# Performance work log

Measured on AMD Instinct MI355X. Metric: run time of the kernel, lower is better.

The kernel has to match this reference:

```python
import jax, jax.numpy as jnp
import numpy as np

B, M, N, T = 16, 16, 32, 80


def setup_inputs() -> dict:
    key = jax.random.key(0)
    ks = jax.random.split(key, 20)
    p = lambda k, shp: jax.random.normal(k, shp, jnp.float32) * 0.05
    return {
        "ego_traj": jax.random.normal(ks[0], (B, M, T, 6), jnp.float32),
        "ego_encoding": jax.random.normal(ks[1], (B, 256), jnp.float32),
        "agents_traj": jax.random.normal(ks[2], (B, M, N, T, 3), jnp.float32),
        "agents_states": jax.random.normal(ks[3], (B, N, 11), jnp.float32),
        # interaction_feature_encoder: Linear(10,64) -> ReLU -> Linear(64,256)
        "enc_w1": p(ks[4], (10, 64)), "enc_b1": p(ks[5], (64,)),
        "enc_w2": p(ks[6], (64, 256)), "enc_b2": p(ks[7], (256,)),
        # interaction_feature_decoder: Linear(256,64) -> ELU -> Linear(64,4) -> Sigmoid
        "dec_w1": p(ks[8], (256, 64)), "dec_b1": p(ks[9], (64,)),
        "dec_w2": p(ks[10], (64, 4)), "dec_b2": p(ks[11], (4,)),
        # weights_decoder: Linear(256,64) -> ELU -> Linear(64,8) -> Softplus
        "wd_w1": p(ks[12], (256, 64)), "wd_b1": p(ks[13], (64,)),
        "wd_w2": p(ks[14], (64, 8)), "wd_b2": p(ks[15], (8,)),
        "timesteps": 80,
    }


def reference(ego_traj, ego_encoding, agents_traj, agents_states,
              enc_w1, enc_b1, enc_w2, enc_b2,
              dec_w1, dec_b1, dec_w2, dec_b2,
              wd_w1, wd_b1, wd_w2, wd_b2, timesteps):
    Tm = timesteps
    # ---- hardcoded ego features: B,M,4 ----
    speed = ego_traj[:, :, :Tm, 3]
    acc = ego_traj[:, :, :Tm, 4]
    jerk = jnp.diff(acc, axis=-1) / 0.1
    jerk = jnp.concatenate([jerk[:, :, :1], jerk], axis=-1)
    curvature = ego_traj[:, :, :Tm, 5]
    lat_acc = speed ** 2 * curvature
    hard = jnp.stack([
        -jnp.clip(speed.mean(-1), 0.0, 15.0) / 15.0,
        jnp.clip(jnp.abs(acc).mean(-1), 0.0, 4.0) / 4.0,
        jnp.clip(jnp.abs(jerk).mean(-1), 0.0, 6.0) / 6.0,
        jnp.clip(jnp.abs(lat_acc).mean(-1), 0.0, 5.0) / 5.0,
    ], axis=-1)  # B,M,4

    # ---- latent interaction features (vectorized over M) ----
    agent_mask = (agents_states.sum(-1) != 0).astype(ego_traj.dtype)  # B,N
    ry = agents_traj[:, :, :, :Tm, 2] - ego_traj[:, :, None, :Tm, 2]  # B,M,N,T
    ry = jnp.arctan2(jnp.sin(ry), jnp.cos(ry))
    rp = agents_traj[:, :, :, :Tm, :2] - ego_traj[:, :, None, :Tm, :2]
    rp = jnp.stack([rp[..., 0] * jnp.cos(ry), rp[..., 1] * jnp.sin(ry)], axis=-1)
    av = jnp.diff(agents_traj[:, :, :, :Tm, :2], axis=-2) / 0.1
    av = jnp.concatenate([av[:, :, :, :1, :], av], axis=-2)
    evx = ego_traj[:, :, :Tm, 3] * jnp.cos(ego_traj[:, :, :Tm, 2])  # B,M,T
    evy = ego_traj[:, :, :Tm, 3] * jnp.sin(ego_traj[:, :, :Tm, 2])
    rv = jnp.stack([(av[..., 0] - evx[:, :, None]) * jnp.cos(ry),
                    (av[..., 1] - evy[:, :, None]) * jnp.sin(ry)], axis=-1)
    rel = jnp.concatenate([rp, ry[..., None], rv], axis=-1)  # B,M,N,T,5
    aattr = jnp.broadcast_to(agents_states[:, None, :, None, 6:], rel.shape[:4] + (5,))
    attr = jnp.concatenate([rel, aattr], axis=-1) * agent_mask[:, None, :, None, None]  # B,M,N,T,10
    h = jax.nn.relu(attr @ enc_w1 + enc_b1) @ enc_w2 + enc_b2  # B,M,N,T,256
    feat = h.max(axis=2).mean(axis=2)  # max over agents, mean over time -> B,M,256
    inter = jax.nn.sigmoid(jax.nn.elu(feat @ dec_w1 + dec_b1) @ dec_w2 + dec_b2)  # B,M,4

    # ---- weights (variable_cost=False -> ones_like encoding) ----
    enc_in = jnp.ones_like(ego_encoding)
    weights = jax.nn.softplus(jax.nn.elu(enc_in @ wd_w1 + wd_b1) @ wd_w2 + wd_b2)  # B,8

    # ---- collision cost: B,M ----
    dist = jnp.linalg.norm(ego_traj[:, :, None, :Tm, :2] - agents_traj[:, :, :, :Tm, :2], axis=-1)
    coll = (jnp.exp(-0.2 * dist ** 2) * agent_mask[:, None, :, None]).sum((-1, -2))

    feats = jnp.concatenate([hard, inter], axis=-1)  # B,M,8
    scores = -jnp.sum(feats * weights[:, None, :], axis=-1) - 10.0 * coll
    ego_mask = ego_traj.sum(-1).sum(-1) != 0  # B,M
    scores = jnp.where(ego_mask, scores, -jnp.inf)
    return scores, weights
```

## Files before the change

### kernel.cpp

```cpp
#include <hip/hip_runtime.h>
#include <hip/hip_fp16.h>
#include <math.h>
#include <string.h>

typedef __attribute__((ext_vector_type(8))) short short8;
typedef __attribute__((ext_vector_type(8))) _Float16 f16x8;
typedef __attribute__((ext_vector_type(4))) _Float16 h4;
typedef __attribute__((ext_vector_type(2))) _Float16 h2;
typedef __attribute__((ext_vector_type(4))) float f32x4;

#define NB 16
#define NM 16
#define NN 32
#define NT 80
#define TC 16
#define NP 5
#define CH 4
#define NCH 8

#define WS_WTS 0
#define WS_BF 16
#define WS_BB 8208
#define WS_BASE 24592
#define WS_BM_STRIDE 1344
#define WS_SC_OFF 1280

__device__ __forceinline__ short f2h(float f) {
  _Float16 h = (_Float16)f;
  short s; memcpy(&s, &h, 2); return s;
}
__device__ __forceinline__ unsigned h2bits(h2 h) {
  unsigned u; memcpy(&u, &h, 4); return u;
}
__device__ __forceinline__ h2 bits2h(unsigned u) {
  h2 h; memcpy(&h, &u, 4); return h;
}

__global__ void prep_kernel(const float* __restrict__ agents_states,
                            const float* __restrict__ enc_w1,
                            const float* __restrict__ enc_b1,
                            const float* __restrict__ enc_w2,
                            const float* __restrict__ wd_w1,
                            const float* __restrict__ wd_b1,
                            const float* __restrict__ wd_w2,
                            const float* __restrict__ wd_b2,
                            float* __restrict__ ws,
                            float* __restrict__ out) {
  const int blk = blockIdx.x;
  const int tid = threadIdx.x;
  if (blk < NB) {
    __shared__ float smask[NN];
    if (tid < NN) {
      const float* st = agents_states + ((size_t)blk * NN + tid) * 11;
      float s = 0.f;
      for (int i = 0; i < 11; ++i) s += st[i];
      smask[tid] = (s != 0.f) ? 1.f : 0.f;
    }
    __syncthreads();
    h2* bb = reinterpret_cast<h2*>(ws + WS_BB) + blk * (NN * 32);
    for (int e = tid; e < NN * 32; e += 256) {
      int n = e >> 5, jp = e & 31;
      const float* st = agents_states + ((size_t)blk * NN + n) * 11 + 6;
      float v[2];
#pragma unroll
      for (int hh = 0; hh < 2; ++hh) {
        int j = jp * 2 + hh;
        float acc = st[0] * enc_w1[5 * 64 + j] + st[1] * enc_w1[6 * 64 + j] +
                    st[2] * enc_w1[7 * 64 + j] + st[3] * enc_w1[8 * 64 + j] +
                    st[4] * enc_w1[9 * 64 + j];
        v[hh] = smask[n] * acc + enc_b1[j];
      }
      h2 r; r[0] = (_Float16)v[0]; r[1] = (_Float16)v[1];
      bb[e] = r;
    }
  } else {
    __shared__ float sh[64];
    if (tid < 64) {
      float acc = wd_b1[tid];
      for (int i = 0; i < 256; ++i) acc += wd_w1[i * 64 + tid];
      sh[tid] = acc > 0.f ? acc : expm1f(acc);
    }
    __syncthreads();
    if (tid < 8) {
      float acc = wd_b2[tid];
      for (int k = 0; k < 64; ++k) acc += sh[k] * wd_w2[k * 8 + tid];
      float sp = log1pf(__expf(acc));
      ws[WS_WTS + tid] = sp;
      for (int b = 0; b < NB; ++b) out[NB * NM + b * 8 + tid] = sp;
    }
    const int g = tid >> 6;
    const int lane = tid & 63;
    short8* bft = reinterpret_cast<short8*>(ws + WS_BF);
#pragma unroll
    for (int q = 0; q < 8; ++q) {
      int s = g * 8 + q;
      int wv = s >> 3, jb = (s >> 1) & 3, kt = s & 1;
      int col = wv * 64 + jb * 16 + (lane & 15);
      int krow = (lane >> 4) * 8;
      short8 v;
#pragma unroll
      for (int j = 0; j < 8; ++j)
        v[j] = f2h(enc_w2[(kt * 32 + krow + j) * 256 + col]);
      bft[s * 64 + lane] = v;
    }
  }
}

__global__ __launch_bounds__(256, 4) void score_partial(
    const float* __restrict__ ego_traj,
    const float* __restrict__ agents_traj,
    const float* __restrict__ agents_states,
    const float* __restrict__ enc_w1,
    float* __restrict__ ws)
{
  __shared__ h4 s_r01[NN][TC];
  __shared__ h4 s_r23[NN][TC];
  __shared__ h2 s_r4[NN][TC];
  __shared__ uint2 s_bb[NN][16];
  __shared__ __align__(16) char s_hid[2][CH][TC * 128];
  __shared__ float s_ego[TC][5];
  __shared__ float s_acc[TC + 2];
  __shared__ float s_spd[TC], s_lat[TC], s_egos[TC];
  __shared__ float s_mask[NN];
  __shared__ float s_cw[4];

  const int p = blockIdx.x;
  const int bm = blockIdx.y;
  const int t0 = p * TC;
  const int b = bm >> 4;
  const int tid = threadIdx.x;
  const int lane = tid & 63;
  const int wv = tid >> 6;

  float* ws_bm = ws + WS_BASE + (size_t)bm * WS_BM_STRIDE;

  if (tid < TC) {
    int i = tid;
    const float* e = ego_traj + ((size_t)bm * NT + (t0 + i)) * 6;
    float ex = e[0], ey = e[1], eh = e[2], spd = e[3], acc = e[4], cur = e[5];
    s_ego[i][0] = ex; s_ego[i][1] = ey; s_ego[i][2] = eh;
    s_ego[i][3] = spd * __cosf(eh);
    s_ego[i][4] = spd * __sinf(eh);
    s_spd[i] = spd;
    s_acc[i + 1] = acc;
    s_lat[i] = fabsf(spd * spd * cur);
    s_egos[i] = ex + ey + eh + spd + acc + cur;
  } else if (tid == TC) {
    int tp = (p == 0) ? 0 : (t0 - 1);
    s_acc[0] = ego_traj[((size_t)bm * NT + tp) * 6 + 4];
  } else if (tid >= 64 && tid < 64 + NN) {
    int n = tid - 64;
    const float* st = agents_states + ((size_t)b * NN + n) * 11;
    float s = 0.f;
    for (int i = 0; i < 11; ++i) s += st[i];
    s_mask[n] = (s != 0.f) ? 1.f : 0.f;
  }
  {
    const uint2* bbt = reinterpret_cast<const uint2*>(ws + WS_BB) + b * 512;
#pragma unroll
    for (int k = 0; k < 2; ++k) {
      int e = tid + k * 256;
      s_bb[e >> 4][e & 15] = bbt[e];
    }
  }

  const int jq = tid & 15;
  const int tt = tid >> 4;
  const int j0 = jq * 4;

  f16x8 Bf[4][2];
  {
    const f16x8* bft = reinterpret_cast<const f16x8*>(ws + WS_BF);
#pragma unroll
    for (int jb = 0; jb < 4; ++jb)
#pragma unroll
      for (int kt = 0; kt < 2; ++kt)
        Bf[jb][kt] = bft[((wv * 4 + jb) * 2 + kt) * 64 + lane];
  }

  h2 w1h[5][2];
#pragma unroll
  for (int f = 0; f < 5; ++f)
#pragma unroll
    for (int jp = 0; jp < 2; ++jp) {
      h2 r;
      r[0] = (_Float16)enc_w1[f * 64 + j0 + jp * 2];
      r[1] = (_Float16)enc_w1[f * 64 + j0 + jp * 2 + 1];
      w1h[f][jp] = r;
    }
  __syncthreads();

  {
    float collacc = 0.f;
    const float* atraj = agents_traj + (size_t)bm * (NN * NT * 3);
#pragma unroll
    for (int k = 0; k < 2; ++k) {
      int pp = tid + k * 256;
      int n = pp >> 4;
      int i = pp & 15;
      int tg = t0 + i;
      const float* bp = atraj + n * (NT * 3) + tg * 3;
      float ax = bp[0], ay = bp[1], ah = bp[2];
      float avx, avy;
      if (tg == 0) { avx = (bp[3] - ax) * 10.f; avy = (bp[4] - ay) * 10.f; }
      else         { avx = (ax - bp[-3]) * 10.f; avy = (ay - bp[-2]) * 10.f; }
      float ex = s_ego[i][0], ey = s_ego[i][1], eh = s_ego[i][2];
      float evx = s_ego[i][3], evy = s_ego[i][4];
      float m = s_mask[n];
      float ryr = ah - eh;
      float w = ryr - 6.283185307179586f * rintf(ryr * 0.15915494309189535f);
      float cy = __cosf(ryr), sy = __sinf(ryr);
      float dx = ax - ex, dy = ay - ey;
      float r0 = dx * cy * m, r1 = dy * sy * m, r2 = w * m;
      float r3 = (avx - evx) * cy * m, r4 = (avy - evy) * sy * m;
      h4 v01, v23; h2 v4;
      v01[0] = v01[1] = (_Float16)r0; v01[2] = v01[3] = (_Float16)r1;
      v23[0] = v23[1] = (_Float16)r2; v23[2] = v23[3] = (_Float16)r3;
      v4[0] = v4[1] = (_Float16)r4;
      s_r01[n][i] = v01;
      s_r23[n][i] = v23;
      s_r4[n][i] = v4;
      collacc += __expf(-0.2f * (dx * dx + dy * dy)) * m;
    }
#pragma unroll
    for (int off = 1; off < 64; off <<= 1) collacc += __shfl_xor(collacc, off);
    if (lane == 0) s_cw[wv] = collacc;
  }

  if (tid >= 251) {
    int which = tid - 251;
    float s = 0.f;
    if (which == 0)      { for (int i = 0; i < TC; ++i) s += s_spd[i]; }
    else if (which == 1) { for (int i = 0; i < TC; ++i) s += fabsf(s_acc[i + 1]); }
    else if (which == 2) {
      for (int i = 0; i < TC; ++i) {
        int ia = (p == 0 && i == 0) ? 2 : (i + 1);
        s += fabsf((s_acc[ia] - s_acc[ia - 1]) * 10.f);
      }
    }
    else if (which == 3) { for (int i = 0; i < TC; ++i) s += s_lat[i]; }
    else                 { for (int i = 0; i < TC; ++i) s += s_egos[i]; }
    ws_bm[WS_SC_OFF + p * 8 + which] = s;
  }

  const int tl = lane & 15, kg = lane >> 4;
  const int swr = (tl & 7) << 4;
  const int aoff0 = tl * 128 + ((kg * 16) ^ swr);
  const int aoff1 = tl * 128 + ((64 + kg * 16) ^ swr);
  const int wbyte = tt * 128 + ((jq * 8) ^ ((tt & 7) << 4));

  h2 z2; z2[0] = z2[1] = (_Float16)0.f;

  auto compute_chunk = [&](int c, int buf) {
#pragma unroll
    for (int nn = 0; nn < CH; ++nn) {
      const int n = c * CH + nn;
      h4 r01 = s_r01[n][tt];
      h4 r23 = s_r23[n][tt];
      h2 r4 = s_r4[n][tt];
      uint2 bb = s_bb[n][jq];
      h2 a0 = __builtin_shufflevector(r01, r01, 0, 1);
      h2 a1 = __builtin_shufflevector(r01, r01, 2, 3);
      h2 a2 = __builtin_shufflevector(r23, r23, 0, 1);
      h2 a3 = __builtin_shufflevector(r23, r23, 2, 3);
      uint2 u;
#pragma unroll
      for (int jp = 0; jp < 2; ++jp) {
        h2 ha = bits2h(jp ? bb.y : bb.x);
        ha = a0 * w1h[0][jp] + ha;
        ha = a1 * w1h[1][jp] + ha;
        ha = a2 * w1h[2][jp] + ha;
        ha = a3 * w1h[3][jp] + ha;
        ha = r4 * w1h[4][jp] + ha;
        ha = __builtin_elementwise_max(ha, z2);
        if (jp == 0) u.x = h2bits(ha); else u.y = h2bits(ha);
      }
      *reinterpret_cast<uint2*>(&s_hid[buf][nn][0] + wbyte) = u;
    }
  };

  f32x4 rmax[4];
#pragma unroll
  for (int jb = 0; jb < 4; ++jb)
    rmax[jb] = f32x4{-3e38f, -3e38f, -3e38f, -3e38f};

  auto mfma_step = [&](int buf) {
#pragma unroll
    for (int nn = 0; nn < CH; ++nn) {
      const char* slab = &s_hid[buf][nn][0];
      f16x8 A0 = *reinterpret_cast<const f16x8*>(slab + aoff0);
      f16x8 A1 = *reinterpret_cast<const f16x8*>(slab + aoff1);
#pragma unroll
      for (int jb = 0; jb < 4; ++jb) {
        f32x4 c = {0.f, 0.f, 0.f, 0.f};
        c = __builtin_amdgcn_mfma_f32_16x16x32_f16(A0, Bf[jb][0], c, 0, 0, 0);
        c = __builtin_amdgcn_mfma_f32_16x16x32_f16(A1, Bf[jb][1], c, 0, 0, 0);
        rmax[jb] = __builtin_elementwise_max(rmax[jb], c);
      }
    }
  };

  __syncthreads();
  compute_chunk(0, 0);
  __syncthreads();

  for (int c = 0; c < NCH; ++c) {
    if (c + 1 < NCH) compute_chunk(c + 1, (c + 1) & 1);
    mfma_step(c & 1);
    __syncthreads();
  }

  {
#pragma unroll
    for (int jb = 0; jb < 4; ++jb) {
      float s = (rmax[jb][0] + rmax[jb][1]) + (rmax[jb][2] + rmax[jb][3]);
      s += __shfl_xor(s, 16);
      s += __shfl_xor(s, 32);
      if (lane < 16)
        ws_bm[p * 256 + wv * 64 + jb * 16 + lane] = s;
    }
  }
  if (tid == 0)
    ws_bm[WS_SC_OFF + p * 8 + 5] = s_cw[0] + s_cw[1] + s_cw[2] + s_cw[3];
}

__global__ void combine_kernel(const float* __restrict__ ws,
                               const float* __restrict__ enc_b2,
                               const float* __restrict__ dec_w1,
                               const float* __restrict__ dec_b1,
                               const float* __restrict__ dec_w2,
                               const float* __restrict__ dec_b2,
                               float* __restrict__ out_scores) {
  __shared__ float s_feat[256];
  __shared__ float s_dh[64];
  __shared__ float s_hard[4];
  __shared__ float s_inter[4];
  __shared__ float s_mc[2];
  const int bm = blockIdx.x;
  const int tid = threadIdx.x;
  const float* wb = ws + WS_BASE + (size_t)bm * WS_BM_STRIDE;

  for (int c = tid; c < 256; c += 64) {
    float f = 0.f;
#pragma unroll
    for (int pp = 0; pp < NP; ++pp) f += wb[pp * 256 + c];
    s_feat[c] = f * (1.f / NT) + enc_b2[c];
  }
  const float* sc = wb + WS_SC_OFF;
  if (tid < 6) {
    float s = 0.f;
#pragma unroll
    for (int pp = 0; pp < NP; ++pp) s += sc[pp * 8 + tid];
    if (tid == 0) s_hard[0] = -fminf(fmaxf(s * (1.f / NT), 0.f), 15.f) * (1.f / 15.f);
    if (tid == 1) s_hard[1] = fminf(fmaxf(s * (1.f / NT), 0.f), 4.f) * 0.25f;
    if (tid == 2) s_hard[2] = fminf(fmaxf(s * (1.f / NT), 0.f), 6.f) * (1.f / 6.f);
    if (tid == 3) s_hard[3] = fminf(fmaxf(s * (1.f / NT), 0.f), 5.f) * 0.2f;
    if (tid == 4) s_mc[0] = s;
    if (tid == 5) s_mc[1] = s;
  }
  __syncthreads();

  {
    float a0 = 0.f, a1 = 0.f, a2 = 0.f, a3 = 0.f;
    for (int i = 0; i < 256; i += 4) {
      a0 += s_feat[i + 0] * dec_w1[(i + 0) * 64 + tid];
      a1 += s_feat[i + 1] * dec_w1[(i + 1) * 64 + tid];
      a2 += s_feat[i + 2] * dec_w1[(i + 2) * 64 + tid];
      a3 += s_feat[i + 3] * dec_w1[(i + 3) * 64 + tid];
    }
    float acc = dec_b1[tid] + ((a0 + a1) + (a2 + a3));
    s_dh[tid] = acc > 0.f ? acc : expm1f(acc);
  }
  __syncthreads();

  if (tid < 4) {
    float acc = dec_b2[tid];
    for (int k = 0; k < 64; ++k) acc += s_dh[k] * dec_w2[k * 4 + tid];
    s_inter[tid] = 1.f / (1.f + __expf(-acc));
  }
  __syncthreads();

  if (tid == 0) {
    const float* wts = ws + WS_WTS;
    float scv = 0.f;
#pragma unroll
    for (int i = 0; i < 4; ++i) scv += s_hard[i] * wts[i];
#pragma unroll
    for (int i = 0; i < 4; ++i) scv += s_inter[i] * wts[4 + i];
    scv = -scv - 10.f * s_mc[1];
    if (s_mc[0] == 0.f) scv = -INFINITY;
    out_scores[bm] = scv;
  }
}

extern "C" void kernel_launch(void* const* d_in, const int* in_sizes, int n_in,
                              void* d_out, int out_size, void* d_ws, size_t ws_size,
                              hipStream_t stream) {
  const float* ego_traj      = (const float*)d_in[0];
  const float* agents_traj   = (const float*)d_in[2];
  const float* agents_states = (const float*)d_in[3];
  const float* enc_w1 = (const float*)d_in[4];
  const float* enc_b1 = (const float*)d_in[5];
  const float* enc_w2 = (const float*)d_in[6];
  const float* enc_b2 = (const float*)d_in[7];
  const float* dec_w1 = (const float*)d_in[8];
  const float* dec_b1 = (const float*)d_in[9];
  const float* dec_w2 = (const float*)d_in[10];
  const float* dec_b2 = (const float*)d_in[11];
  const float* wd_w1 = (const float*)d_in[12];
  const float* wd_b1 = (const float*)d_in[13];
  const float* wd_w2 = (const float*)d_in[14];
  const float* wd_b2 = (const float*)d_in[15];

  float* out = (float*)d_out;
  float* ws = (float*)d_ws;

  prep_kernel<<<NB + 1, 256, 0, stream>>>(agents_states, enc_w1, enc_b1, enc_w2,
                                          wd_w1, wd_b1, wd_w2, wd_b2, ws, out);
  dim3 grid(NP, NB * NM);
  score_partial<<<grid, 256, 0, stream>>>(
      ego_traj, agents_traj, agents_states, enc_w1, ws);
  combine_kernel<<<NB * NM, 64, 0, stream>>>(
      ws, enc_b2, dec_w1, dec_b1, dec_w2, dec_b2, out);
}
```

Baseline: 43.26 us.

## Fuse combine into score kernel via last-block atomic counter; split weight prep

Removes the separate combine kernel launch. Each (b,m) row now has a counter in the workspace that prep zeroes. The last score block to finish for a row runs the decoder MLP and writes the score, reusing shared memory and splitting the 256x64 matvec across four waves. The fp16 repacking of enc_w2 also moves from one prep block into eight extra blocks to shorten the prep critical path. The cost is an atomic, threadfences and a serial tail inside the last block of each row.

```diff
diff --git a/kernel.cpp b/kernel.cpp
--- a/kernel.cpp
+++ b/kernel.cpp
@@ -19,9 +19,10 @@
 #define NCH 8
 
 #define WS_WTS 0
-#define WS_BF 16
-#define WS_BB 8208
-#define WS_BASE 24592
+#define WS_CNT 8
+#define WS_BF 264
+#define WS_BB 8456
+#define WS_BASE 24840
 #define WS_BM_STRIDE 1344
 #define WS_SC_OFF 1280
 
@@ -49,6 +50,8 @@
   const int blk = blockIdx.x;
   const int tid = threadIdx.x;
   if (blk < NB) {
+    if (tid < 16)
+      reinterpret_cast<unsigned*>(ws + WS_CNT)[blk * 16 + tid] = 0u;
     __shared__ float smask[NN];
     if (tid < NN) {
       const float* st = agents_states + ((size_t)blk * NN + tid) * 11;
@@ -73,6 +76,18 @@
       h2 r; r[0] = (_Float16)v[0]; r[1] = (_Float16)v[1];
       bb[e] = r;
     }
+  } else if (blk < NB + 8) {
+    const int g = tid >> 6;
+    const int lane = tid & 63;
+    const int s = (blk - NB) * 4 + g;
+    const int wv = s >> 3, jb = (s >> 1) & 3, kt = s & 1;
+    const int col = wv * 64 + jb * 16 + (lane & 15);
+    const int krow = (lane >> 4) * 8;
+    short8 v;
+#pragma unroll
+    for (int j = 0; j < 8; ++j)
+      v[j] = f2h(enc_w2[(kt * 32 + krow + j) * 256 + col]);
+    reinterpret_cast<short8*>(ws + WS_BF)[s * 64 + lane] = v;
   } else {
     __shared__ float sh[64];
     if (tid < 64) {
@@ -88,21 +103,6 @@
       ws[WS_WTS + tid] = sp;
       for (int b = 0; b < NB; ++b) out[NB * NM + b * 8 + tid] = sp;
     }
-    const int g = tid >> 6;
-    const int lane = tid & 63;
-    short8* bft = reinterpret_cast<short8*>(ws + WS_BF);
-#pragma unroll
-    for (int q = 0; q < 8; ++q) {
-      int s = g * 8 + q;
-      int wv = s >> 3, jb = (s >> 1) & 3, kt = s & 1;
-      int col = wv * 64 + jb * 16 + (lane & 15);
-      int krow = (lane >> 4) * 8;
-      short8 v;
-#pragma unroll
-      for (int j = 0; j < 8; ++j)
-        v[j] = f2h(enc_w2[(kt * 32 + krow + j) * 256 + col]);
-      bft[s * 64 + lane] = v;
-    }
   }
 }
 
@@ -111,7 +111,11 @@
     const float* __restrict__ agents_traj,
     const float* __restrict__ agents_states,
     const float* __restrict__ enc_w1,
-    float* __restrict__ ws)
+    const float* __restrict__ enc_b2,
+    const float* __restrict__ dec_w1, const float* __restrict__ dec_b1,
+    const float* __restrict__ dec_w2, const float* __restrict__ dec_b2,
+    float* __restrict__ ws,
+    float* __restrict__ out_scores)
 {
   __shared__ h4 s_r01[NN][TC];
   __shared__ h4 s_r23[NN][TC];
@@ -123,6 +127,8 @@
   __shared__ float s_spd[TC], s_lat[TC], s_egos[TC];
   __shared__ float s_mask[NN];
   __shared__ float s_cw[4];
+  __shared__ int s_last;
+  __shared__ float s_hard[4], s_inter[4], s_mc[2];
 
   const int p = blockIdx.x;
   const int bm = blockIdx.y;
@@ -133,6 +139,7 @@
   const int wv = tid >> 6;
 
   float* ws_bm = ws + WS_BASE + (size_t)bm * WS_BM_STRIDE;
+  unsigned* cnt_bm = reinterpret_cast<unsigned*>(ws + WS_CNT) + bm;
 
   if (tid < TC) {
     int i = tid;
@@ -322,64 +329,62 @@
   }
   if (tid == 0)
     ws_bm[WS_SC_OFF + p * 8 + 5] = s_cw[0] + s_cw[1] + s_cw[2] + s_cw[3];
-}
-
-__global__ void combine_kernel(const float* __restrict__ ws,
-                               const float* __restrict__ enc_b2,
-                               const float* __restrict__ dec_w1,
-                               const float* __restrict__ dec_b1,
-                               const float* __restrict__ dec_w2,
-                               const float* __restrict__ dec_b2,
-                               float* __restrict__ out_scores) {
-  __shared__ float s_feat[256];
-  __shared__ float s_dh[64];
-  __shared__ float s_hard[4];
-  __shared__ float s_inter[4];
-  __shared__ float s_mc[2];
-  const int bm = blockIdx.x;
-  const int tid = threadIdx.x;
-  const float* wb = ws + WS_BASE + (size_t)bm * WS_BM_STRIDE;
-
-  for (int c = tid; c < 256; c += 64) {
-    float f = 0.f;
-#pragma unroll
-    for (int pp = 0; pp < NP; ++pp) f += wb[pp * 256 + c];
+
+  __syncthreads();
+  if (tid == 0) {
+    __threadfence();
+    unsigned old = atomicAdd(cnt_bm, 1u);
+    s_last = (old == NP - 1) ? 1 : 0;
+  }
+  __syncthreads();
+  if (!s_last) return;
+  __threadfence();
+
+  float* s_feat = reinterpret_cast<float*>(&s_r01[0][0]);
+  float* s_dhp  = reinterpret_cast<float*>(&s_r23[0][0]);
+  float* s_dh   = reinterpret_cast<float*>(&s_r4[0][0]);
+
+  {
+    volatile const float* wb = ws + WS_BASE + (size_t)bm * WS_BM_STRIDE;
+    int c = tid;
+    float f = wb[c] + wb[256 + c] + wb[512 + c] + wb[768 + c] + wb[1024 + c];
     s_feat[c] = f * (1.f / NT) + enc_b2[c];
-  }
-  const float* sc = wb + WS_SC_OFF;
-  if (tid < 6) {
-    float s = 0.f;
-#pragma unroll
-    for (int pp = 0; pp < NP; ++pp) s += sc[pp * 8 + tid];
-    if (tid == 0) s_hard[0] = -fminf(fmaxf(s * (1.f / NT), 0.f), 15.f) * (1.f / 15.f);
-    if (tid == 1) s_hard[1] = fminf(fmaxf(s * (1.f / NT), 0.f), 4.f) * 0.25f;
-    if (tid == 2) s_hard[2] = fminf(fmaxf(s * (1.f / NT), 0.f), 6.f) * (1.f / 6.f);
-    if (tid == 3) s_hard[3] = fminf(fmaxf(s * (1.f / NT), 0.f), 5.f) * 0.2f;
-    if (tid == 4) s_mc[0] = s;
-    if (tid == 5) s_mc[1] = s;
-  }
-  __syncthreads();
-
-  {
-    float a0 = 0.f, a1 = 0.f, a2 = 0.f, a3 = 0.f;
-    for (int i = 0; i < 256; i += 4) {
-      a0 += s_feat[i + 0] * dec_w1[(i + 0) * 64 + tid];
-      a1 += s_feat[i + 1] * dec_w1[(i + 1) * 64 + tid];
-      a2 += s_feat[i + 2] * dec_w1[(i + 2) * 64 + tid];
-      a3 += s_feat[i + 3] * dec_w1[(i + 3) * 64 + tid];
-    }
-    float acc = dec_b1[tid] + ((a0 + a1) + (a2 + a3));
+    if (tid < 6) {
+      volatile const float* sc = wb + WS_SC_OFF;
+      float s = 0.f;
+#pragma unroll
+      for (int pp = 0; pp < NP; ++pp) s += sc[pp * 8 + tid];
+      if (tid == 0) s_hard[0] = -fminf(fmaxf(s * (1.f / NT), 0.f), 15.f) * (1.f / 15.f);
+      if (tid == 1) s_hard[1] = fminf(fmaxf(s * (1.f / NT), 0.f), 4.f) * 0.25f;
+      if (tid == 2) s_hard[2] = fminf(fmaxf(s * (1.f / NT), 0.f), 6.f) * (1.f / 6.f);
+      if (tid == 3) s_hard[3] = fminf(fmaxf(s * (1.f / NT), 0.f), 5.f) * 0.2f;
+      if (tid == 4) s_mc[0] = s;
+      if (tid == 5) s_mc[1] = s;
+    }
+  }
+  __syncthreads();
+
+  {
+    const int q = tid >> 6, j = tid & 63;
+    float a = 0.f;
+#pragma unroll 8
+    for (int i = 0; i < 64; ++i)
+      a += s_feat[q * 64 + i] * dec_w1[(q * 64 + i) * 64 + j];
+    s_dhp[q * 64 + j] = a;
+  }
+  __syncthreads();
+  if (tid < 64) {
+    float acc = dec_b1[tid] + ((s_dhp[tid] + s_dhp[64 + tid]) +
+                               (s_dhp[128 + tid] + s_dhp[192 + tid]));
     s_dh[tid] = acc > 0.f ? acc : expm1f(acc);
   }
   __syncthreads();
-
   if (tid < 4) {
     float acc = dec_b2[tid];
     for (int k = 0; k < 64; ++k) acc += s_dh[k] * dec_w2[k * 4 + tid];
     s_inter[tid] = 1.f / (1.f + __expf(-acc));
   }
   __syncthreads();
-
   if (tid == 0) {
     const float* wts = ws + WS_WTS;
     float scv = 0.f;
@@ -415,11 +420,10 @@
   float* out = (float*)d_out;
   float* ws = (float*)d_ws;
 
-  prep_kernel<<<NB + 1, 256, 0, stream>>>(agents_states, enc_w1, enc_b1, enc_w2,
+  prep_kernel<<<NB + 9, 256, 0, stream>>>(agents_states, enc_w1, enc_b1, enc_w2,
                                           wd_w1, wd_b1, wd_w2, wd_b2, ws, out);
   dim3 grid(NP, NB * NM);
   score_partial<<<grid, 256, 0, stream>>>(
-      ego_traj, agents_traj, agents_states, enc_w1, ws);
-  combine_kernel<<<NB * NM, 64, 0, stream>>>(
-      ws, enc_b2, dec_w1, dec_b1, dec_w2, dec_b2, out);
-}
+      ego_traj, agents_traj, agents_states, enc_w1, enc_b2,
+      dec_w1, dec_b1, dec_w2, dec_b2, ws, out);
+}
```

Result: slower. 109.9 us (+154.1%).
